# Performance work log

Measured on AMD Instinct MI355X. Metric: run time of the kernel, lower is better.

## Reference

```python
import jax, jax.numpy as jnp
import numpy as np

# ---- static config ----
G = 4          # num graphs
NG = 512       # nodes per graph
N = G * NG     # total nodes
E = 32768      # num edges
IN_DIM = 128
HID = 32
HEADS = 4
HC = HID * HEADS  # 128
OUT_DIM = 32
N_LAYERS = 2
GRID = 500
Q = 20
NEG_SLOPE = 0.2
QUANTILES = jnp.asarray(np.linspace(0.0, 1.0, Q), jnp.float32)  # [Q]


def setup_inputs() -> dict:
    key = jax.random.key(0)
    ks = jax.random.split(key, 32)
    inp = {}
    inp['x'] = jax.random.normal(ks[0], (N, IN_DIM), jnp.float32)
    inp['edge_index'] = jax.random.randint(ks[1], (2, E), 0, N).astype(jnp.int64)
    inp['batch'] = (jnp.arange(N) // NG).astype(jnp.int64)
    # GATConv params (2 layers, both 128 -> 4 heads x 32, concat)
    for l, (kin,) in enumerate([(IN_DIM,), (HC,)]):
        s = 1.0 / np.sqrt(kin)
        inp[f'W{l}'] = jax.random.normal(ks[2 + 4 * l], (kin, HC), jnp.float32) * s
        inp[f'as{l}'] = jax.random.normal(ks[3 + 4 * l], (HEADS, HID), jnp.float32) * s
        inp[f'ad{l}'] = jax.random.normal(ks[4 + 4 * l], (HEADS, HID), jnp.float32) * s
        inp[f'b{l}'] = jnp.zeros((HC,), jnp.float32)
    for l in range(N_LAYERS + 1):
        inp[f'lpW{l}'] = jax.random.normal(ks[10 + 2 * l], (HC, OUT_DIM), jnp.float32) * (1.0 / np.sqrt(HC))
        inp[f'lpb{l}'] = jnp.zeros((OUT_DIM,), jnp.float32)
    for l in range(N_LAYERS + 1):
        inp[f'kW{l}'] = jax.random.normal(ks[16 + 2 * l], (HC * Q, OUT_DIM), jnp.float32) * (1.0 / np.sqrt(HC * Q))
        inp[f'kb{l}'] = jnp.zeros((OUT_DIM,), jnp.float32)
    inp['pool_w'] = jnp.ones((2,), jnp.float32) / 2.0
    inp['beta'] = jax.random.normal(ks[22], (OUT_DIM,), jnp.float32)
    inp['h0'] = jax.random.normal(ks[23], (1,), jnp.float32)
    return inp


def _gat_layer(x, src, dst, W, a_src, a_dst, bias):
    # PyG GATConv (concat=True, add_self_loops=True, negative_slope=0.2), eval mode
    n = x.shape[0]
    xh = (x @ W).reshape(n, HEADS, HID)              # [N,H,C]
    loop = jnp.arange(n)
    s = jnp.concatenate([src, loop])                 # [E+N]
    d = jnp.concatenate([dst, loop])
    al_s = jnp.einsum('nhc,hc->nh', xh, a_src)       # [N,H]
    al_d = jnp.einsum('nhc,hc->nh', xh, a_dst)
    e = jax.nn.leaky_relu(al_s[s] + al_d[d], NEG_SLOPE)   # [E+N,H]
    e_max = jax.ops.segment_max(e, d, num_segments=n)     # stable softmax per dst
    e = jnp.exp(e - e_max[d])
    denom = jax.ops.segment_sum(e, d, num_segments=n)
    alpha = e / (denom[d] + 1e-16)                   # [E+N,H]
    out = jax.ops.segment_sum(alpha[:, :, None] * xh[s], d, num_segments=n)
    return out.reshape(n, HC) + bias


def _kde_per_graph(xg):
    # xg: [Ng, D] -> [D*Q] soft-quantile features via grid KDE
    n = xg.shape[0]
    mn = xg.min(axis=0) - 1e-6                       # [D]
    mx = xg.max(axis=0) + 1e-6
    grid = jnp.linspace(0.0, 1.0, GRID)[:, None] * (mx - mn) + mn   # [Gp,D]
    std = xg.std(axis=0) + 1e-8 / 3
    h = 1.06 * std * float(n) ** (-0.2)              # [D]
    u = (grid[:, None, :] - xg[None, :, :]) / h      # [Gp,Ng,D]  (dominant tensor)
    kern = jnp.exp(-0.5 * u * u) / (h * np.sqrt(2.0 * np.pi))
    density = kern.mean(axis=1)                      # [Gp,D]
    cdf = jnp.cumsum(density, axis=0)
    cdf = cdf / jnp.clip(cdf[-1:], 1e-8)
    dist = jnp.abs(cdf[:, :, None] - QUANTILES)      # [Gp,D,Q]
    w = jax.nn.sigmoid(-100.0 * dist)
    w = w / (w.sum(axis=0, keepdims=True) + 1e-8)
    qv = (grid[:, :, None] * w).sum(axis=0)          # [D,Q]
    return qv.reshape(-1)


def _readout(cur, lpW, lpb, kW, kb, pool_w):
    xr = cur.reshape(G, NG, -1)
    pooled = jnp.stack([xr.mean(axis=1), xr.max(axis=1)], axis=0)   # [2,G,D]
    wp = (pooled * pool_w[:, None, None]).sum(axis=0)               # [G,D]
    h = wp @ lpW + lpb                                              # [G,out]
    kf = jax.vmap(_kde_per_graph)(xr)                               # [G,D*Q]
    return h, kf @ kW + kb


def reference(x, edge_index, batch, W0, as0, ad0, b0, W1, as1, ad1, b1,
              lpW0, lpb0, lpW1, lpb1, lpW2, lpb2,
              kW0, kb0, kW1, kb1, kW2, kb2, pool_w, beta, h0):
    src, dst = edge_index[0], edge_index[1]
    convs = [(W0, as0, ad0, b0), (W1, as1, ad1, b1)]
    lps = [(lpW0, lpb0), (lpW1, lpb1), (lpW2, lpb2)]
    kps = [(kW0, kb0), (kW1, kb1), (kW2, kb2)]
    cur = x
    h_list, kde_list = [], []
    for i in range(N_LAYERS):
        h, kp = _readout(cur, lps[i][0], lps[i][1], kps[i][0], kps[i][1], pool_w)
        h_list.append(h); kde_list.append(kp)
        cur = _gat_layer(cur, src, dst, *convs[i])
        if i != N_LAYERS - 1:
            cur = jax.nn.relu(cur)
    h, kp = _readout(cur, lps[-1][0], lps[-1][1], kps[-1][0], kps[-1][1], pool_w)
    h_list.append(h); kde_list.append(kp)
    main_out = jnp.stack(h_list).mean(axis=0)        # [G,out]
    kde_out = jnp.stack(kde_list).mean(axis=0)
    risk = (main_out + kde_out) @ beta + h0          # [G]
    return risk
```

## Files before the change

### kernel.cpp

```cpp
#include <hip/hip_runtime.h>
#include <math.h>

#define GNUM 4
#define NG 512
#define NN 2048
#define EE 32768
#define HC 128
#define HEADS 4
#define HID 32
#define GRID_PTS 500
#define QN 20
#define ODIM 32
#define MAXE 160

#define LOG2E 1.44269504088896340736f
#define NEG_HALF_LOG2E -0.72134752044448170368f
#define N_POW_M02 0.2871745887492588f
#define SIG_K 144.269504089f

__device__ __forceinline__ float fexp2(float x){ return __builtin_amdgcn_exp2f(x); }
__device__ __forceinline__ float frcp(float x){ return __builtin_amdgcn_rcpf(x); }

struct SmemKDE {
  float4 wred4[8];
  float sc[4];
  float wsum[8], woff[9];
  float redw[QN][8], redg[QN][8];
  float qs[QN];
};
struct SmemXW  { float rows[4][HC]; int cnt[4]; };
struct SmemGat {
  int   ssrc[4][MAXE];
  float sexp[4][MAXE][HEADS];
};
union Smem { SmemKDE kde; SmemXW xw; SmemGat gat; };

__device__ void kde_phase(Smem& sm, const float* __restrict__ curT,
        const float* __restrict__ kW, const float* __restrict__ kb, float* __restrict__ kacc,
        const float* __restrict__ lpW, const float* __restrict__ lpb,
        const float* __restrict__ poolw, float* __restrict__ macc){
  int b = blockIdx.x;
  int g = b >> 7, d = b & 127;
  int t = threadIdx.x;
  int lane = t & 63, wave = t >> 6;
  float2 vv = ((const float2*)curT)[(size_t)d*NN + g*NG + t];
  float v = vv.x, v2 = vv.y;
  float mn=v, mx=v, smv=v, sq=v2;
  #pragma unroll
  for (int m=32; m>0; m>>=1){
    mn = fminf(mn, __shfl_xor(mn, m, 64));
    mx = fmaxf(mx, __shfl_xor(mx, m, 64));
    smv += __shfl_xor(smv, m, 64);
    sq += __shfl_xor(sq, m, 64);
  }
  if (lane==0) sm.kde.wred4[wave] = make_float4(mn,mx,smv,sq);
  __syncthreads();
  if (t==0){
    float4 r = sm.kde.wred4[0];
    #pragma unroll
    for (int i=1;i<8;++i){
      float4 bb = sm.kde.wred4[i];
      r.x = fminf(r.x,bb.x); r.y = fmaxf(r.y,bb.y); r.z += bb.z; r.w += bb.w;
    }
    float mean = r.z * (1.f/NG);
    float var  = fmaxf(r.w*(1.f/NG) - mean*mean, 0.f);
    float sd   = sqrtf(var) + (1e-8f/3.f);
    float h    = 1.06f * sd * N_POW_M02;
    float lo = r.x - 1e-6f, hi = r.y + 1e-6f;
    sm.kde.sc[0] = lo;
    sm.kde.sc[1] = (hi-lo)*(1.f/(GRID_PTS-1));
    sm.kde.sc[2] = NEG_HALF_LOG2E/(h*h);
    sm.kde.sc[3] = poolw[0]*mean + poolw[1]*r.y;
  }
  __syncthreads();
  float lo = sm.kde.sc[0], st = sm.kde.sc[1], kk = sm.kde.sc[2];
  float gv = lo + st*(float)t;
  float acc = 0.f;
  {
    float c0 = kk*gv*gv, c1 = -2.f*kk*gv;
    const float4* p4 = (const float4*)curT + (((size_t)d*NN + g*NG) >> 1);
    #pragma unroll 4
    for (int i=0;i<NG/2;++i){
      float4 s2 = p4[i];
      acc += fexp2(fmaf(kk, s2.y, fmaf(c1, s2.x, c0)));
      acc += fexp2(fmaf(kk, s2.w, fmaf(c1, s2.z, c0)));
    }
  }
  if (t >= GRID_PTS) acc = 0.f;
  float sv = acc;
  #pragma unroll
  for (int off=1; off<64; off<<=1){
    float n = __shfl_up(sv, off, 64);
    if (lane >= off) sv += n;
  }
  if (lane==63) sm.kde.wsum[wave] = sv;
  __syncthreads();
  if (t==0){
    float r2 = 0.f;
    #pragma unroll
    for (int i=0;i<8;++i){ sm.kde.woff[i]=r2; r2+=sm.kde.wsum[i]; }
    sm.kde.woff[8]=r2;
  }
  if (t < QN*8){ ((float*)sm.kde.redw)[t]=0.f; ((float*)sm.kde.redg)[t]=0.f; }
  __syncthreads();
  float invt = 1.f/fmaxf(sm.kde.woff[8], 1e-8f);
  float c = (sv + sm.kde.woff[wave]) * invt;
  float cw0 = __shfl(c, 0, 64), cw1 = __shfl(c, 63, 64);
  int qlo = max(0, (int)ceilf((cw0 - 0.17f)*(float)(QN-1)));
  int qhi = min(QN-1, (int)floorf((cw1 + 0.17f)*(float)(QN-1)));
  for (int q=qlo; q<=qhi; ++q){
    float w = 0.f;
    if (t < GRID_PTS){
      float dist = fabsf(c - (float)q*(1.f/(QN-1)));
      w = frcp(1.f + fexp2(SIG_K*dist));
    }
    float gw = gv*w;
    #pragma unroll
    for (int m=32;m>0;m>>=1){
      w  += __shfl_xor(w,  m, 64);
      gw += __shfl_xor(gw, m, 64);
    }
    if (lane==0){ sm.kde.redw[q][wave]=w; sm.kde.redg[q][wave]=gw; }
  }
  __syncthreads();
  if (t < QN){
    float sw=0.f, sgw=0.f;
    #pragma unroll
    for (int i=0;i<8;++i){ sw+=sm.kde.redw[t][i]; sgw+=sm.kde.redg[t][i]; }
    sm.kde.qs[t] = sgw / (sw + 1e-8f);
  }
  __syncthreads();
  if (t < ODIM){
    float a = 0.f;
    const float* kwb = kW + (size_t)d*QN*ODIM + t;
    #pragma unroll
    for (int q=0;q<QN;++q) a += sm.kde.qs[q]*kwb[q*ODIM];
    if (d==0) a += kb[t];
    kacc[(size_t)d*128 + g*ODIM + t] = a;
    float bb = sm.kde.sc[3]*lpW[d*ODIM + t];
    if (d==0) bb += lpb[t];
    macc[(size_t)d*128 + g*ODIM + t] = bb;
  }
  __syncthreads();
}

__device__ float gather_core(Smem& sm, int d, int sub, int tl,
        const int* __restrict__ csr, const int* __restrict__ deg,
        const float* __restrict__ als, const float* __restrict__ ald,
        const float* __restrict__ xh, const float* __restrict__ bias){
  int dg = deg[d];
  int E = dg + 1;
  int Ep = (E + 7) & ~7;
  const int* base = csr + d*MAXE;
  float a0 = ald[d*4+0], a1 = ald[d*4+1], a2 = ald[d*4+2], a3 = ald[d*4+3];
  for (int i=tl; i<Ep; i+=128){
    int s = (i < dg) ? base[i] : d;
    sm.gat.ssrc[sub][i] = s;
    if (i < E){
      float e0 = als[s*4+0]+a0, e1 = als[s*4+1]+a1, e2 = als[s*4+2]+a2, e3 = als[s*4+3]+a3;
      e0 = (e0>=0.f)? e0 : 0.2f*e0;
      e1 = (e1>=0.f)? e1 : 0.2f*e1;
      e2 = (e2>=0.f)? e2 : 0.2f*e2;
      e3 = (e3>=0.f)? e3 : 0.2f*e3;
      sm.gat.sexp[sub][i][0]=e0; sm.gat.sexp[sub][i][1]=e1;
      sm.gat.sexp[sub][i][2]=e2; sm.gat.sexp[sub][i][3]=e3;
    } else {
      sm.gat.sexp[sub][i][0]=0.f; sm.gat.sexp[sub][i][1]=0.f;
      sm.gat.sexp[sub][i][2]=0.f; sm.gat.sexp[sub][i][3]=0.f;
    }
  }
  __syncthreads();
  int h = tl >> 5, l32 = tl & 31;
  float mx = -INFINITY;
  for (int i=l32; i<E; i+=32) mx = fmaxf(mx, sm.gat.sexp[sub][i][h]);
  #pragma unroll
  for (int m=16; m>0; m>>=1) mx = fmaxf(mx, __shfl_xor(mx, m, 32));
  float sdn = 0.f;
  for (int i=l32; i<E; i+=32){
    float ev = fexp2(LOG2E*(sm.gat.sexp[sub][i][h] - mx));
    sm.gat.sexp[sub][i][h] = ev;
    sdn += ev;
  }
  #pragma unroll
  for (int m=16; m>0; m>>=1) sdn += __shfl_xor(sdn, m, 32);
  float fac = 1.f/(sdn + 1e-16f);
  float acc = bias[tl];
  for (int i0=0; i0<Ep; i0+=8){
    #pragma unroll
    for (int k=0;k<8;++k){
      int i = i0 + k;
      acc += sm.gat.sexp[sub][i][h]*fac * xh[(size_t)sm.gat.ssrc[sub][i]*HC + tl];
    }
  }
  __syncthreads();
  return acc;
}

__device__ void xw_emit(Smem& sm, int sub, int j, int n,
        const float* __restrict__ W, const float* __restrict__ as_, const float* __restrict__ ad_,
        float* __restrict__ xh, float* __restrict__ als, float* __restrict__ ald){
  float acc = 0.f;
  #pragma unroll 8
  for (int c2=0;c2<HC;++c2)
    acc += sm.xw.rows[sub][c2]*W[(size_t)c2*HC + j];
  xh[(size_t)n*HC + j] = acc;
  int h = j >> 5, cc = j & 31;
  float ps = acc*as_[h*HID+cc], pd = acc*ad_[h*HID+cc];
  #pragma unroll
  for (int m=16;m>0;m>>=1){
    ps += __shfl_xor(ps, m, 32);
    pd += __shfl_xor(pd, m, 32);
  }
  if (cc==0){ als[n*HEADS+h]=ps; ald[n*HEADS+h]=pd; }
}

__device__ void write_transposed(Smem& sm, int t, int n0, float* __restrict__ curT){
  if (t < HC){
    float v0 = sm.xw.rows[0][t], v1 = sm.xw.rows[1][t];
    float v2 = sm.xw.rows[2][t], v3 = sm.xw.rows[3][t];
    float4* p = (float4*)(curT + (((size_t)t*NN + n0) << 1));
    p[0] = make_float4(v0, v0*v0, v1, v1*v1);
    p[1] = make_float4(v2, v2*v2, v3, v3*v3);
  }
}

__global__ __launch_bounds__(512) void k_T(const float* __restrict__ x, float* __restrict__ xT){
  __shared__ float rows[4][HC];
  int t = threadIdx.x;
  int sub = t >> 7, j = t & 127;
  int n0 = blockIdx.x*4;
  rows[sub][j] = x[(size_t)(n0+sub)*HC + j];
  __syncthreads();
  if (t < HC){
    float v0 = rows[0][t], v1 = rows[1][t], v2 = rows[2][t], v3 = rows[3][t];
    float4* p = (float4*)(xT + (((size_t)t*NN + n0) << 1));
    p[0] = make_float4(v0, v0*v0, v1, v1*v1);
    p[1] = make_float4(v2, v2*v2, v3, v3*v3);
  }
}

__global__ __launch_bounds__(512) void k_L0(const float* __restrict__ x, const float* __restrict__ xT,
        const float* __restrict__ kW, const float* __restrict__ kb, float* __restrict__ kacc,
        const float* __restrict__ lpW, const float* __restrict__ lpb,
        const float* __restrict__ poolw, float* __restrict__ macc,
        const float* __restrict__ W, const float* __restrict__ as_, const float* __restrict__ ad_,
        float* __restrict__ xh, float* __restrict__ als, float* __restrict__ ald,
        const int* __restrict__ src, const int* __restrict__ dst,
        int* __restrict__ deg, int* __restrict__ csr){
  __shared__ Smem sm;
  int t = threadIdx.x;
  if (blockIdx.x < 512){
    kde_phase(sm, xT, kW, kb, kacc, lpW, lpb, poolw, macc);
  } else {
    int b2 = blockIdx.x - 512;
    int sub = t >> 7, j = t & 127;
    int n = b2*4 + sub;
    if (t < 4) sm.xw.cnt[t] = 0;
    sm.xw.rows[sub][j] = x[(size_t)n*HC + j];
    __syncthreads();
    int base4 = b2*4;
    for (int e = t; e < EE; e += 512){
      int dd = dst[e];
      unsigned r = (unsigned)(dd - base4);
      if (r < 4u){
        int p = atomicAdd(&sm.xw.cnt[r], 1);
        if (p < MAXE) csr[dd*MAXE + p] = src[e];
      }
    }
    xw_emit(sm, sub, j, n, W, as_, ad_, xh, als, ald);
    __syncthreads();
    if (t < 4) deg[base4 + t] = min(sm.xw.cnt[t], MAXE-1);
  }
}

__global__ __launch_bounds__(512) void k_G0(const int* __restrict__ csr, const int* __restrict__ deg,
        const float* __restrict__ als_in, const float* __restrict__ ald_in,
        const float* __restrict__ xh_in, const float* __restrict__ bias,
        float* __restrict__ cur1T,
        const float* __restrict__ W1, const float* __restrict__ as1, const float* __restrict__ ad1,
        float* __restrict__ xh2, float* __restrict__ als2, float* __restrict__ ald2){
  __shared__ Smem sm;
  int t = threadIdx.x;
  int sub = t >> 7, tl = t & 127;
  int d = blockIdx.x*4 + sub;
  float acc = gather_core(sm, d, sub, tl, csr, deg, als_in, ald_in, xh_in, bias);
  sm.xw.rows[sub][tl] = fmaxf(acc, 0.f);
  __syncthreads();
  write_transposed(sm, t, blockIdx.x*4, cur1T);
  xw_emit(sm, sub, tl, d, W1, as1, ad1, xh2, als2, ald2);
}

__global__ __launch_bounds__(512) void k_L1(const float* __restrict__ cur1T,
        const float* __restrict__ kW, const float* __restrict__ kb, float* __restrict__ kacc,
        const float* __restrict__ lpW, const float* __restrict__ lpb,
        const float* __restrict__ poolw, float* __restrict__ macc,
        const int* __restrict__ csr, const int* __restrict__ deg,
        const float* __restrict__ als2, const float* __restrict__ ald2,
        const float* __restrict__ xh2, const float* __restrict__ bias,
        float* __restrict__ cur2T){
  __shared__ Smem sm;
  int t = threadIdx.x;
  if (blockIdx.x < 512){
    kde_phase(sm, cur1T, kW, kb, kacc, lpW, lpb, poolw, macc);
  } else {
    int b2 = blockIdx.x - 512;
    int sub = t >> 7, tl = t & 127;
    int d = b2*4 + sub;
    float acc = gather_core(sm, d, sub, tl, csr, deg, als2, ald2, xh2, bias);
    sm.xw.rows[sub][tl] = acc;
    __syncthreads();
    write_transposed(sm, t, b2*4, cur2T);
  }
}

__global__ __launch_bounds__(512) void k_L2(const float* __restrict__ cur2T,
        const float* __restrict__ kW, const float* __restrict__ kb, float* __restrict__ kacc,
        const float* __restrict__ lpW, const float* __restrict__ lpb,
        const float* __restrict__ poolw, float* __restrict__ macc){
  __shared__ Smem sm;
  kde_phase(sm, cur2T, kW, kb, kacc, lpW, lpb, poolw, macc);
}

__global__ __launch_bounds__(384) void k_final(const float* __restrict__ mpart, const float* __restrict__ kpart,
                        const float* __restrict__ beta, const float* __restrict__ h0,
                        float* __restrict__ out){
  int t = threadIdx.x;
  __shared__ float sdm[384];
  int l = t >> 7, tt = t & 127;
  const float* mrow = mpart + (size_t)l*16384 + tt;
  const float* krow = kpart + (size_t)l*16384 + tt;
  float s = 0.f;
  #pragma unroll 8
  for (int d2=0; d2<128; ++d2) s += mrow[(size_t)d2*128] + krow[(size_t)d2*128];
  sdm[t] = s;
  __syncthreads();
  if (t < 128){
    int g = t >> 5, o = t & 31;
    float s3 = (sdm[t] + sdm[t+128] + sdm[t+256]) * (1.f/3.f) * beta[o];
    #pragma unroll
    for (int m=16; m>0; m>>=1) s3 += __shfl_xor(s3, m, 32);
    if (o == 0) out[g] = s3 + h0[0];
  }
}

extern "C" void kernel_launch(void* const* d_in, const int* in_sizes, int n_in,
                              void* d_out, int out_size, void* d_ws, size_t ws_size,
                              hipStream_t stream) {
  (void)in_sizes; (void)n_in; (void)out_size; (void)ws_size;
  const float* x    = (const float*)d_in[0];
  const int*   ei   = (const int*)d_in[1];
  const int*   srcp = ei;
  const int*   dstp = ei + EE;
  const float* W[2]   = {(const float*)d_in[3], (const float*)d_in[7]};
  const float* As[2]  = {(const float*)d_in[4], (const float*)d_in[8]};
  const float* Ad[2]  = {(const float*)d_in[5], (const float*)d_in[9]};
  const float* Bi[2]  = {(const float*)d_in[6], (const float*)d_in[10]};
  const float* lpW[3] = {(const float*)d_in[11], (const float*)d_in[13], (const float*)d_in[15]};
  const float* lpb[3] = {(const float*)d_in[12], (const float*)d_in[14], (const float*)d_in[16]};
  const float* kW[3]  = {(const float*)d_in[17], (const float*)d_in[19], (const float*)d_in[21]};
  const float* kb[3]  = {(const float*)d_in[18], (const float*)d_in[20], (const float*)d_in[22]};
  const float* poolw  = (const float*)d_in[23];
  const float* beta   = (const float*)d_in[24];
  const float* h0     = (const float*)d_in[25];
  float* out = (float*)d_out;

  float* ws = (float*)d_ws;
  float* cur1T = ws;
  float* cur2T = cur1T + 524288;
  float* xT    = cur2T + 524288;
  float* xh    = xT + 524288;
  float* xh2   = xh + 262144;
  float* als   = xh2 + 262144;
  float* ald   = als + 8192;
  float* als2  = ald + 8192;
  float* ald2  = als2 + 8192;
  float* mpart = ald2 + 8192;
  float* kpart = mpart + 49152;
  int*   deg   = (int*)(kpart + 49152);
  int*   csr   = deg + 2048;

  k_T<<<512, 512, 0, stream>>>(x, xT);
  k_L0<<<1024, 512, 0, stream>>>(x, xT, kW[0], kb[0], kpart, lpW[0], lpb[0], poolw, mpart,
                                 W[0], As[0], Ad[0], xh, als, ald,
                                 srcp, dstp, deg, csr);
  k_G0<<<512, 512, 0, stream>>>(csr, deg, als, ald, xh, Bi[0], cur1T,
                                W[1], As[1], Ad[1], xh2, als2, ald2);
  k_L1<<<1024, 512, 0, stream>>>(cur1T, kW[1], kb[1], kpart+16384, lpW[1], lpb[1], poolw, mpart+16384,
                                 csr, deg, als2, ald2, xh2, Bi[1], cur2T);
  k_L2<<<512, 512, 0, stream>>>(cur2T, kW[2], kb[2], kpart+32768, lpW[2], lpb[2], poolw, mpart+32768);
  k_final<<<1, 384, 0, stream>>>(mpart, kpart, beta, h0, out);
}
```

Measured before the change: 214.1 us.

## Split KDE layer-0 work across two kernels and use planar value/square layout

The interleaved value/square transposed buffers become two separate planes, and the KDE inner loop uses packed 2-wide FMAs over float4 loads from each plane. The layer-0 KDE blocks are now split. Half run in k_L0 after the xw/CSR blocks, which are placed first. The other half run alongside the first gather kernel in k_G0. This aims to balance the work and overlap the KDE with graph work, at the cost of a larger launch for k_G0 and two load streams per KDE iteration.

New measurement: 213.2 us. Within noise of the previous version (-0.4%).

```diff
diff --git a/kernel.cpp b/kernel.cpp
--- a/kernel.cpp
+++ b/kernel.cpp
@@ -17,6 +17,8 @@
 #define NEG_HALF_LOG2E -0.72134752044448170368f
 #define N_POW_M02 0.2871745887492588f
 #define SIG_K 144.269504089f
+
+typedef float v2f __attribute__((ext_vector_type(2)));
 
 __device__ __forceinline__ float fexp2(float x){ return __builtin_amdgcn_exp2f(x); }
 __device__ __forceinline__ float frcp(float x){ return __builtin_amdgcn_rcpf(x); }
@@ -35,16 +37,17 @@
 };
 union Smem { SmemKDE kde; SmemXW xw; SmemGat gat; };
 
-__device__ void kde_phase(Smem& sm, const float* __restrict__ curT,
+__device__ void kde_phase(Smem& sm, const float* __restrict__ vpl, const float* __restrict__ spl,
+        int b,
         const float* __restrict__ kW, const float* __restrict__ kb, float* __restrict__ kacc,
         const float* __restrict__ lpW, const float* __restrict__ lpb,
         const float* __restrict__ poolw, float* __restrict__ macc){
-  int b = blockIdx.x;
   int g = b >> 7, d = b & 127;
   int t = threadIdx.x;
   int lane = t & 63, wave = t >> 6;
-  float2 vv = ((const float2*)curT)[(size_t)d*NN + g*NG + t];
-  float v = vv.x, v2 = vv.y;
+  size_t base = (size_t)d*NN + g*NG;
+  float v  = vpl[base + t];
+  float v2 = spl[base + t];
   float mn=v, mx=v, smv=v, sq=v2;
   #pragma unroll
   for (int m=32; m>0; m>>=1){
@@ -78,12 +81,21 @@
   float acc = 0.f;
   {
     float c0 = kk*gv*gv, c1 = -2.f*kk*gv;
-    const float4* p4 = (const float4*)curT + (((size_t)d*NN + g*NG) >> 1);
-    #pragma unroll 4
-    for (int i=0;i<NG/2;++i){
-      float4 s2 = p4[i];
-      acc += fexp2(fmaf(kk, s2.y, fmaf(c1, s2.x, c0)));
-      acc += fexp2(fmaf(kk, s2.w, fmaf(c1, s2.z, c0)));
+    v2f c0v = {c0, c0}, c1v = {c1, c1}, kkv = {kk, kk};
+    const float4* pv = (const float4*)(vpl + base);
+    const float4* ps = (const float4*)(spl + base);
+    #pragma unroll 8
+    for (int i=0;i<NG/4;++i){
+      float4 a = pv[i];
+      float4 bq = ps[i];
+      v2f alo = {a.x, a.y}, ahi = {a.z, a.w};
+      v2f blo = {bq.x, bq.y}, bhi = {bq.z, bq.w};
+      v2f plo = __builtin_elementwise_fma(kkv, blo, __builtin_elementwise_fma(c1v, alo, c0v));
+      v2f phi = __builtin_elementwise_fma(kkv, bhi, __builtin_elementwise_fma(c1v, ahi, c0v));
+      acc += fexp2(plo.x);
+      acc += fexp2(plo.y);
+      acc += fexp2(phi.x);
+      acc += fexp2(phi.y);
     }
   }
   if (t >= GRID_PTS) acc = 0.f;
@@ -214,17 +226,18 @@
   if (cc==0){ als[n*HEADS+h]=ps; ald[n*HEADS+h]=pd; }
 }
 
-__device__ void write_transposed(Smem& sm, int t, int n0, float* __restrict__ curT){
+__device__ void write_transposed(Smem& sm, int t, int n0,
+                                 float* __restrict__ vpl, float* __restrict__ spl){
   if (t < HC){
     float v0 = sm.xw.rows[0][t], v1 = sm.xw.rows[1][t];
     float v2 = sm.xw.rows[2][t], v3 = sm.xw.rows[3][t];
-    float4* p = (float4*)(curT + (((size_t)t*NN + n0) << 1));
-    p[0] = make_float4(v0, v0*v0, v1, v1*v1);
-    p[1] = make_float4(v2, v2*v2, v3, v3*v3);
-  }
-}
-
-__global__ __launch_bounds__(512) void k_T(const float* __restrict__ x, float* __restrict__ xT){
+    *(float4*)(vpl + (size_t)t*NN + n0) = make_float4(v0, v1, v2, v3);
+    *(float4*)(spl + (size_t)t*NN + n0) = make_float4(v0*v0, v1*v1, v2*v2, v3*v3);
+  }
+}
+
+__global__ __launch_bounds__(512) void k_T(const float* __restrict__ x,
+                                           float* __restrict__ vpl, float* __restrict__ spl){
   __shared__ float rows[4][HC];
   int t = threadIdx.x;
   int sub = t >> 7, j = t & 127;
@@ -233,13 +246,13 @@
   __syncthreads();
   if (t < HC){
     float v0 = rows[0][t], v1 = rows[1][t], v2 = rows[2][t], v3 = rows[3][t];
-    float4* p = (float4*)(xT + (((size_t)t*NN + n0) << 1));
-    p[0] = make_float4(v0, v0*v0, v1, v1*v1);
-    p[1] = make_float4(v2, v2*v2, v3, v3*v3);
-  }
-}
-
-__global__ __launch_bounds__(512) void k_L0(const float* __restrict__ x, const float* __restrict__ xT,
+    *(float4*)(vpl + (size_t)t*NN + n0) = make_float4(v0, v1, v2, v3);
+    *(float4*)(spl + (size_t)t*NN + n0) = make_float4(v0*v0, v1*v1, v2*v2, v3*v3);
+  }
+}
+
+__global__ __launch_bounds__(512) void k_L0(const float* __restrict__ x,
+        const float* __restrict__ xTv, const float* __restrict__ xTs,
         const float* __restrict__ kW, const float* __restrict__ kb, float* __restrict__ kacc,
         const float* __restrict__ lpW, const float* __restrict__ lpb,
         const float* __restrict__ poolw, float* __restrict__ macc,
@@ -249,10 +262,10 @@
         int* __restrict__ deg, int* __restrict__ csr){
   __shared__ Smem sm;
   int t = threadIdx.x;
-  if (blockIdx.x < 512){
-    kde_phase(sm, xT, kW, kb, kacc, lpW, lpb, poolw, macc);
+  if (blockIdx.x >= 512){
+    kde_phase(sm, xTv, xTs, blockIdx.x - 512, kW, kb, kacc, lpW, lpb, poolw, macc);
   } else {
-    int b2 = blockIdx.x - 512;
+    int b2 = blockIdx.x;
     int sub = t >> 7, j = t & 127;
     int n = b2*4 + sub;
     if (t < 4) sm.xw.cnt[t] = 0;
@@ -276,32 +289,40 @@
 __global__ __launch_bounds__(512) void k_G0(const int* __restrict__ csr, const int* __restrict__ deg,
         const float* __restrict__ als_in, const float* __restrict__ ald_in,
         const float* __restrict__ xh_in, const float* __restrict__ bias,
-        float* __restrict__ cur1T,
+        float* __restrict__ c1v, float* __restrict__ c1s,
         const float* __restrict__ W1, const float* __restrict__ as1, const float* __restrict__ ad1,
-        float* __restrict__ xh2, float* __restrict__ als2, float* __restrict__ ald2){
+        float* __restrict__ xh2, float* __restrict__ als2, float* __restrict__ ald2,
+        const float* __restrict__ xTv, const float* __restrict__ xTs,
+        const float* __restrict__ kW, const float* __restrict__ kb, float* __restrict__ kacc,
+        const float* __restrict__ lpW, const float* __restrict__ lpb,
+        const float* __restrict__ poolw, float* __restrict__ macc){
   __shared__ Smem sm;
   int t = threadIdx.x;
+  if (blockIdx.x >= 512){
+    kde_phase(sm, xTv, xTs, blockIdx.x - 256, kW, kb, kacc, lpW, lpb, poolw, macc);
+    return;
+  }
   int sub = t >> 7, tl = t & 127;
   int d = blockIdx.x*4 + sub;
   float acc = gather_core(sm, d, sub, tl, csr, deg, als_in, ald_in, xh_in, bias);
   sm.xw.rows[sub][tl] = fmaxf(acc, 0.f);
   __syncthreads();
-  write_transposed(sm, t, blockIdx.x*4, cur1T);
+  write_transposed(sm, t, blockIdx.x*4, c1v, c1s);
   xw_emit(sm, sub, tl, d, W1, as1, ad1, xh2, als2, ald2);
 }
 
-__global__ __launch_bounds__(512) void k_L1(const float* __restrict__ cur1T,
+__global__ __launch_bounds__(512) void k_L1(const float* __restrict__ c1v, const float* __restrict__ c1s,
         const float* __restrict__ kW, const float* __restrict__ kb, float* __restrict__ kacc,
         const float* __restrict__ lpW, const float* __restrict__ lpb,
         const float* __restrict__ poolw, float* __restrict__ macc,
         const int* __restrict__ csr, const int* __restrict__ deg,
         const float* __restrict__ als2, const float* __restrict__ ald2,
         const float* __restrict__ xh2, const float* __restrict__ bias,
-        float* __restrict__ cur2T){
+        float* __restrict__ c2v, float* __restrict__ c2s){
   __shared__ Smem sm;
   int t = threadIdx.x;
   if (blockIdx.x < 512){
-    kde_phase(sm, cur1T, kW, kb, kacc, lpW, lpb, poolw, macc);
+    kde_phase(sm, c1v, c1s, blockIdx.x, kW, kb, kacc, lpW, lpb, poolw, macc);
   } else {
     int b2 = blockIdx.x - 512;
     int sub = t >> 7, tl = t & 127;
@@ -309,16 +330,16 @@
     float acc = gather_core(sm, d, sub, tl, csr, deg, als2, ald2, xh2, bias);
     sm.xw.rows[sub][tl] = acc;
     __syncthreads();
-    write_transposed(sm, t, b2*4, cur2T);
-  }
-}
-
-__global__ __launch_bounds__(512) void k_L2(const float* __restrict__ cur2T,
+    write_transposed(sm, t, b2*4, c2v, c2s);
+  }
+}
+
+__global__ __launch_bounds__(512) void k_L2(const float* __restrict__ c2v, const float* __restrict__ c2s,
         const float* __restrict__ kW, const float* __restrict__ kb, float* __restrict__ kacc,
         const float* __restrict__ lpW, const float* __restrict__ lpb,
         const float* __restrict__ poolw, float* __restrict__ macc){
   __shared__ Smem sm;
-  kde_phase(sm, cur2T, kW, kb, kacc, lpW, lpb, poolw, macc);
+  kde_phase(sm, c2v, c2s, blockIdx.x, kW, kb, kacc, lpW, lpb, poolw, macc);
 }
 
 __global__ __launch_bounds__(384) void k_final(const float* __restrict__ mpart, const float* __restrict__ kpart,
@@ -365,10 +386,13 @@
   float* out = (float*)d_out;
 
   float* ws = (float*)d_ws;
-  float* cur1T = ws;
-  float* cur2T = cur1T + 524288;
-  float* xT    = cur2T + 524288;
-  float* xh    = xT + 524288;
+  float* xTv   = ws;
+  float* xTs   = xTv + 262144;
+  float* c1v   = xTs + 262144;
+  float* c1s   = c1v + 262144;
+  float* c2v   = c1s + 262144;
+  float* c2s   = c2v + 262144;
+  float* xh    = c2s + 262144;
   float* xh2   = xh + 262144;
   float* als   = xh2 + 262144;
   float* ald   = als + 8192;
@@ -379,14 +403,15 @@
   int*   deg   = (int*)(kpart + 49152);
   int*   csr   = deg + 2048;
 
-  k_T<<<512, 512, 0, stream>>>(x, xT);
-  k_L0<<<1024, 512, 0, stream>>>(x, xT, kW[0], kb[0], kpart, lpW[0], lpb[0], poolw, mpart,
-                                 W[0], As[0], Ad[0], xh, als, ald,
-                                 srcp, dstp, deg, csr);
-  k_G0<<<512, 512, 0, stream>>>(csr, deg, als, ald, xh, Bi[0], cur1T,
-                                W[1], As[1], Ad[1], xh2, als2, ald2);
-  k_L1<<<1024, 512, 0, stream>>>(cur1T, kW[1], kb[1], kpart+16384, lpW[1], lpb[1], poolw, mpart+16384,
-                                 csr, deg, als2, ald2, xh2, Bi[1], cur2T);
-  k_L2<<<512, 512, 0, stream>>>(cur2T, kW[2], kb[2], kpart+32768, lpW[2], lpb[2], poolw, mpart+32768);
+  k_T<<<512, 512, 0, stream>>>(x, xTv, xTs);
+  k_L0<<<768, 512, 0, stream>>>(x, xTv, xTs, kW[0], kb[0], kpart, lpW[0], lpb[0], poolw, mpart,
+                                W[0], As[0], Ad[0], xh, als, ald,
+                                srcp, dstp, deg, csr);
+  k_G0<<<768, 512, 0, stream>>>(csr, deg, als, ald, xh, Bi[0], c1v, c1s,
+                                W[1], As[1], Ad[1], xh2, als2, ald2,
+                                xTv, xTs, kW[0], kb[0], kpart, lpW[0], lpb[0], poolw, mpart);
+  k_L1<<<1024, 512, 0, stream>>>(c1v, c1s, kW[1], kb[1], kpart+16384, lpW[1], lpb[1], poolw, mpart+16384,
+                                 csr, deg, als2, ald2, xh2, Bi[1], c2v, c2s);
+  k_L2<<<512, 512, 0, stream>>>(c2v, c2s, kW[2], kb[2], kpart+32768, lpW[2], lpb[2], poolw, mpart+32768);
   k_final<<<1, 384, 0, stream>>>(mpart, kpart, beta, h0, out);
 }
```

## Stage KDE samples in shared memory and drop the transpose kernel

Applied to the files above, without the earlier changes.

The KDE phase now loads one value per thread into shared memory and runs the 500-point exponential sum from LDS. Before, each thread streamed the interleaved (v, v²) array from global memory. v² is recomputed with packed float2 FMAs, the sum is split into two accumulators, and layer 0 reads x directly with a strided access. This removes the separate transpose kernel and halves the transposed buffers. It also switches the attention-logit gather to a single float4 load. The costs are an uncoalesced strided read of x in layer 0 and extra ALU work for the squares.

After: 217.1 us. No clear change (+1.4%).

```diff
diff --git a/kernel.cpp b/kernel.cpp
--- a/kernel.cpp
+++ b/kernel.cpp
@@ -18,10 +18,13 @@
 #define N_POW_M02 0.2871745887492588f
 #define SIG_K 144.269504089f
 
+typedef float v2f __attribute__((ext_vector_type(2)));
+
 __device__ __forceinline__ float fexp2(float x){ return __builtin_amdgcn_exp2f(x); }
 __device__ __forceinline__ float frcp(float x){ return __builtin_amdgcn_rcpf(x); }
 
 struct SmemKDE {
+  __align__(16) float xs[NG];
   float4 wred4[8];
   float sc[4];
   float wsum[8], woff[9];
@@ -29,22 +32,21 @@
   float qs[QN];
 };
 struct SmemXW  { float rows[4][HC]; int cnt[4]; };
-struct SmemGat {
-  int   ssrc[4][MAXE];
-  float sexp[4][MAXE][HEADS];
-};
+struct SmemGat { int ssrc[4][MAXE]; float sexp[4][MAXE][HEADS]; };
 union Smem { SmemKDE kde; SmemXW xw; SmemGat gat; };
 
-__device__ void kde_phase(Smem& sm, const float* __restrict__ curT,
+template<int SRC>
+__device__ void kde_phase(Smem& sm, const float* __restrict__ cur, int b,
         const float* __restrict__ kW, const float* __restrict__ kb, float* __restrict__ kacc,
         const float* __restrict__ lpW, const float* __restrict__ lpb,
         const float* __restrict__ poolw, float* __restrict__ macc){
-  int b = blockIdx.x;
   int g = b >> 7, d = b & 127;
   int t = threadIdx.x;
   int lane = t & 63, wave = t >> 6;
-  float2 vv = ((const float2*)curT)[(size_t)d*NN + g*NG + t];
-  float v = vv.x, v2 = vv.y;
+  float v = SRC ? cur[(size_t)d*NN + g*NG + t]
+                : cur[((size_t)g*NG + t)*HC + d];
+  float v2 = v*v;
+  sm.kde.xs[t] = v;
   float mn=v, mx=v, smv=v, sq=v2;
   #pragma unroll
   for (int m=32; m>0; m>>=1){
@@ -75,17 +77,33 @@
   __syncthreads();
   float lo = sm.kde.sc[0], st = sm.kde.sc[1], kk = sm.kde.sc[2];
   float gv = lo + st*(float)t;
-  float acc = 0.f;
+  float accL = 0.f, accH = 0.f;
   {
     float c0 = kk*gv*gv, c1 = -2.f*kk*gv;
-    const float4* p4 = (const float4*)curT + (((size_t)d*NN + g*NG) >> 1);
-    #pragma unroll 4
-    for (int i=0;i<NG/2;++i){
-      float4 s2 = p4[i];
-      acc += fexp2(fmaf(kk, s2.y, fmaf(c1, s2.x, c0)));
-      acc += fexp2(fmaf(kk, s2.w, fmaf(c1, s2.z, c0)));
-    }
-  }
+    v2f c0v = {c0, c0}, c1v = {c1, c1}, kkv = {kk, kk};
+    const float4* p4 = (const float4*)sm.kde.xs;
+    #pragma unroll 8
+    for (int i=0;i<64;++i){
+      float4 s = p4[i];
+      v2f a0 = {s.x, s.y}, a1 = {s.z, s.w};
+      v2f q0 = a0*a0, q1 = a1*a1;
+      v2f p0 = __builtin_elementwise_fma(kkv, q0, __builtin_elementwise_fma(c1v, a0, c0v));
+      v2f p1 = __builtin_elementwise_fma(kkv, q1, __builtin_elementwise_fma(c1v, a1, c0v));
+      accL += fexp2(p0.x); accL += fexp2(p0.y);
+      accL += fexp2(p1.x); accL += fexp2(p1.y);
+    }
+    #pragma unroll 8
+    for (int i=64;i<128;++i){
+      float4 s = p4[i];
+      v2f a0 = {s.x, s.y}, a1 = {s.z, s.w};
+      v2f q0 = a0*a0, q1 = a1*a1;
+      v2f p0 = __builtin_elementwise_fma(kkv, q0, __builtin_elementwise_fma(c1v, a0, c0v));
+      v2f p1 = __builtin_elementwise_fma(kkv, q1, __builtin_elementwise_fma(c1v, a1, c0v));
+      accH += fexp2(p0.x); accH += fexp2(p0.y);
+      accH += fexp2(p1.x); accH += fexp2(p1.y);
+    }
+  }
+  float acc = accL + accH;
   if (t >= GRID_PTS) acc = 0.f;
   float sv = acc;
   #pragma unroll
@@ -157,7 +175,8 @@
     int s = (i < dg) ? base[i] : d;
     sm.gat.ssrc[sub][i] = s;
     if (i < E){
-      float e0 = als[s*4+0]+a0, e1 = als[s*4+1]+a1, e2 = als[s*4+2]+a2, e3 = als[s*4+3]+a3;
+      float4 av = *(const float4*)(als + (size_t)s*4);
+      float e0 = av.x+a0, e1 = av.y+a1, e2 = av.z+a2, e3 = av.w+a3;
       e0 = (e0>=0.f)? e0 : 0.2f*e0;
       e1 = (e1>=0.f)? e1 : 0.2f*e1;
       e2 = (e2>=0.f)? e2 : 0.2f*e2;
@@ -214,32 +233,15 @@
   if (cc==0){ als[n*HEADS+h]=ps; ald[n*HEADS+h]=pd; }
 }
 
-__device__ void write_transposed(Smem& sm, int t, int n0, float* __restrict__ curT){
+__device__ void write_transposed(Smem& sm, int t, int n0, float* __restrict__ vpl){
   if (t < HC){
     float v0 = sm.xw.rows[0][t], v1 = sm.xw.rows[1][t];
     float v2 = sm.xw.rows[2][t], v3 = sm.xw.rows[3][t];
-    float4* p = (float4*)(curT + (((size_t)t*NN + n0) << 1));
-    p[0] = make_float4(v0, v0*v0, v1, v1*v1);
-    p[1] = make_float4(v2, v2*v2, v3, v3*v3);
-  }
-}
-
-__global__ __launch_bounds__(512) void k_T(const float* __restrict__ x, float* __restrict__ xT){
-  __shared__ float rows[4][HC];
-  int t = threadIdx.x;
-  int sub = t >> 7, j = t & 127;
-  int n0 = blockIdx.x*4;
-  rows[sub][j] = x[(size_t)(n0+sub)*HC + j];
-  __syncthreads();
-  if (t < HC){
-    float v0 = rows[0][t], v1 = rows[1][t], v2 = rows[2][t], v3 = rows[3][t];
-    float4* p = (float4*)(xT + (((size_t)t*NN + n0) << 1));
-    p[0] = make_float4(v0, v0*v0, v1, v1*v1);
-    p[1] = make_float4(v2, v2*v2, v3, v3*v3);
-  }
-}
-
-__global__ __launch_bounds__(512) void k_L0(const float* __restrict__ x, const float* __restrict__ xT,
+    *(float4*)(vpl + (size_t)t*NN + n0) = make_float4(v0, v1, v2, v3);
+  }
+}
+
+__global__ __launch_bounds__(512) void k_L0(const float* __restrict__ x,
         const float* __restrict__ kW, const float* __restrict__ kb, float* __restrict__ kacc,
         const float* __restrict__ lpW, const float* __restrict__ lpb,
         const float* __restrict__ poolw, float* __restrict__ macc,
@@ -250,7 +252,7 @@
   __shared__ Smem sm;
   int t = threadIdx.x;
   if (blockIdx.x < 512){
-    kde_phase(sm, xT, kW, kb, kacc, lpW, lpb, poolw, macc);
+    kde_phase<0>(sm, x, blockIdx.x, kW, kb, kacc, lpW, lpb, poolw, macc);
   } else {
     int b2 = blockIdx.x - 512;
     int sub = t >> 7, j = t & 127;
@@ -276,7 +278,7 @@
 __global__ __launch_bounds__(512) void k_G0(const int* __restrict__ csr, const int* __restrict__ deg,
         const float* __restrict__ als_in, const float* __restrict__ ald_in,
         const float* __restrict__ xh_in, const float* __restrict__ bias,
-        float* __restrict__ cur1T,
+        float* __restrict__ c1v,
         const float* __restrict__ W1, const float* __restrict__ as1, const float* __restrict__ ad1,
         float* __restrict__ xh2, float* __restrict__ als2, float* __restrict__ ald2){
   __shared__ Smem sm;
@@ -286,22 +288,22 @@
   float acc = gather_core(sm, d, sub, tl, csr, deg, als_in, ald_in, xh_in, bias);
   sm.xw.rows[sub][tl] = fmaxf(acc, 0.f);
   __syncthreads();
-  write_transposed(sm, t, blockIdx.x*4, cur1T);
+  write_transposed(sm, t, blockIdx.x*4, c1v);
   xw_emit(sm, sub, tl, d, W1, as1, ad1, xh2, als2, ald2);
 }
 
-__global__ __launch_bounds__(512) void k_L1(const float* __restrict__ cur1T,
+__global__ __launch_bounds__(512) void k_L1(const float* __restrict__ c1v,
         const float* __restrict__ kW, const float* __restrict__ kb, float* __restrict__ kacc,
         const float* __restrict__ lpW, const float* __restrict__ lpb,
         const float* __restrict__ poolw, float* __restrict__ macc,
         const int* __restrict__ csr, const int* __restrict__ deg,
         const float* __restrict__ als2, const float* __restrict__ ald2,
         const float* __restrict__ xh2, const float* __restrict__ bias,
-        float* __restrict__ cur2T){
+        float* __restrict__ c2v){
   __shared__ Smem sm;
   int t = threadIdx.x;
   if (blockIdx.x < 512){
-    kde_phase(sm, cur1T, kW, kb, kacc, lpW, lpb, poolw, macc);
+    kde_phase<1>(sm, c1v, blockIdx.x, kW, kb, kacc, lpW, lpb, poolw, macc);
   } else {
     int b2 = blockIdx.x - 512;
     int sub = t >> 7, tl = t & 127;
@@ -309,16 +311,16 @@
     float acc = gather_core(sm, d, sub, tl, csr, deg, als2, ald2, xh2, bias);
     sm.xw.rows[sub][tl] = acc;
     __syncthreads();
-    write_transposed(sm, t, b2*4, cur2T);
-  }
-}
-
-__global__ __launch_bounds__(512) void k_L2(const float* __restrict__ cur2T,
+    write_transposed(sm, t, b2*4, c2v);
+  }
+}
+
+__global__ __launch_bounds__(512) void k_L2(const float* __restrict__ c2v,
         const float* __restrict__ kW, const float* __restrict__ kb, float* __restrict__ kacc,
         const float* __restrict__ lpW, const float* __restrict__ lpb,
         const float* __restrict__ poolw, float* __restrict__ macc){
   __shared__ Smem sm;
-  kde_phase(sm, cur2T, kW, kb, kacc, lpW, lpb, poolw, macc);
+  kde_phase<1>(sm, c2v, blockIdx.x, kW, kb, kacc, lpW, lpb, poolw, macc);
 }
 
 __global__ __launch_bounds__(384) void k_final(const float* __restrict__ mpart, const float* __restrict__ kpart,
@@ -365,10 +367,9 @@
   float* out = (float*)d_out;
 
   float* ws = (float*)d_ws;
-  float* cur1T = ws;
-  float* cur2T = cur1T + 524288;
-  float* xT    = cur2T + 524288;
-  float* xh    = xT + 524288;
+  float* c1v   = ws;
+  float* c2v   = c1v + 262144;
+  float* xh    = c2v + 262144;
   float* xh2   = xh + 262144;
   float* als   = xh2 + 262144;
   float* ald   = als + 8192;
@@ -379,14 +380,13 @@
   int*   deg   = (int*)(kpart + 49152);
   int*   csr   = deg + 2048;
 
-  k_T<<<512, 512, 0, stream>>>(x, xT);
-  k_L0<<<1024, 512, 0, stream>>>(x, xT, kW[0], kb[0], kpart, lpW[0], lpb[0], poolw, mpart,
+  k_L0<<<1024, 512, 0, stream>>>(x, kW[0], kb[0], kpart, lpW[0], lpb[0], poolw, mpart,
                                  W[0], As[0], Ad[0], xh, als, ald,
                                  srcp, dstp, deg, csr);
-  k_G0<<<512, 512, 0, stream>>>(csr, deg, als, ald, xh, Bi[0], cur1T,
+  k_G0<<<512, 512, 0, stream>>>(csr, deg, als, ald, xh, Bi[0], c1v,
                                 W[1], As[1], Ad[1], xh2, als2, ald2);
-  k_L1<<<1024, 512, 0, stream>>>(cur1T, kW[1], kb[1], kpart+16384, lpW[1], lpb[1], poolw, mpart+16384,
-                                 csr, deg, als2, ald2, xh2, Bi[1], cur2T);
-  k_L2<<<512, 512, 0, stream>>>(cur2T, kW[2], kb[2], kpart+32768, lpW[2], lpb[2], poolw, mpart+32768);
+  k_L1<<<1024, 512, 0, stream>>>(c1v, kW[1], kb[1], kpart+16384, lpW[1], lpb[1], poolw, mpart+16384,
+                                 csr, deg, als2, ald2, xh2, Bi[1], c2v);
+  k_L2<<<512, 512, 0, stream>>>(c2v, kW[2], kb[2], kpart+32768, lpW[2], lpb[2], poolw, mpart+32768);
   k_final<<<1, 384, 0, stream>>>(mpart, kpart, beta, h0, out);
 }
```
